# Optimization experiments

Hardware: AMD Instinct MI355X
Metric: run time of the kernel (lower is better)

## Reference

```python
import jax, jax.numpy as jnp
import numpy as np

N_NODES = 150000
N_EDGES = 2400000
IN_DIM, HID, OUT_DIM = 2, 32, 1


def gcn_conv(x, edge_index, W, b, n_nodes):
    """PyG-style GCNConv: add self-loops, sym-normalize, aggregate, linear."""
    h = x @ W  # [N, F_out] linear first (as in PyG GCNConv)
    loop = jnp.arange(n_nodes)
    src = jnp.concatenate([edge_index[0], loop])
    dst = jnp.concatenate([edge_index[1], loop])
    deg = jax.ops.segment_sum(jnp.ones(src.shape[0], h.dtype), dst,
                              num_segments=n_nodes)  # in-degree incl. self-loops
    dinv = jnp.where(deg > 0, jax.lax.rsqrt(deg), 0.0)
    norm = dinv[src] * dinv[dst]  # [E+N]
    msg = h[src] * norm[:, None]  # gather + scale
    out = jax.ops.segment_sum(msg, dst, num_segments=n_nodes)  # scatter-add
    return out + b


def setup_inputs() -> dict:
    key = jax.random.key(0)
    ks = jax.random.split(key, 8)
    x = jax.random.normal(ks[0], (N_NODES, IN_DIM), dtype=jnp.float32)
    edge_index = jax.random.randint(ks[1], (2, N_EDGES), 0, N_NODES, dtype=jnp.int32)
    W1 = jax.random.normal(ks[2], (IN_DIM, HID), dtype=jnp.float32) / np.sqrt(IN_DIM)
    b1 = jnp.zeros((HID,), jnp.float32)
    W2 = jax.random.normal(ks[3], (HID, HID), dtype=jnp.float32) / np.sqrt(HID)
    b2 = jnp.zeros((HID,), jnp.float32)
    Wp = jax.random.normal(ks[4], (HID, OUT_DIM), dtype=jnp.float32) / np.sqrt(HID)
    bp = jnp.zeros((OUT_DIM,), jnp.float32)
    return {"x": x, "edge_index": edge_index, "W1": W1, "b1": b1,
            "W2": W2, "b2": b2, "Wp": Wp, "bp": bp}


def reference(x, edge_index, W1, b1, W2, b2, Wp, bp):
    n = x.shape[0]
    h = jax.nn.relu(gcn_conv(x, edge_index, W1, b1, n))
    h = jax.nn.relu(gcn_conv(h, edge_index, W2, b2, n))
    return jax.nn.sigmoid(h @ Wp + bp)  # [N, 1]
```

## Files before the change

kernel.cpp:

```cpp
#include <hip/hip_runtime.h>

#define HID 32
#define SH 9
#define BNODES 512
#define NBMAX 320
#define TILE 8192

typedef unsigned int uint;

__device__ __forceinline__ uint f2bf(float v) {
    uint b = __float_as_uint(v);
    return (b + 0x7fffu + ((b >> 16) & 1u)) >> 16;
}

__global__ void k_zero(int* __restrict__ p, int n) {
    int i = blockIdx.x * 256 + threadIdx.x;
    if (i < n) p[i] = 0;
}

__global__ void __launch_bounds__(512) k_bcount(const int* __restrict__ dst,
                                                int* __restrict__ bcnt, int E, int NB) {
    __shared__ int c[NBMAX];
    for (int b = threadIdx.x; b < NBMAX; b += 512) c[b] = 0;
    __syncthreads();
    int E4 = E >> 2;
    int b4 = blockIdx.x * (TILE >> 2);
    const int4* dst4 = (const int4*)dst;
#pragma unroll
    for (int k = 0; k < TILE / 4 / 512; ++k) {
        int q = b4 + k * 512 + threadIdx.x;
        if (q < E4) {
            int4 d = dst4[q];
            atomicAdd(&c[d.x >> SH], 1);
            atomicAdd(&c[d.y >> SH], 1);
            atomicAdd(&c[d.z >> SH], 1);
            atomicAdd(&c[d.w >> SH], 1);
        }
    }
    if (blockIdx.x == 0 && threadIdx.x == 0)
        for (int i = E4 << 2; i < E; ++i) atomicAdd(&c[dst[i] >> SH], 1);
    __syncthreads();
    for (int b = threadIdx.x; b < NB; b += 512)
        if (c[b]) atomicAdd(&bcnt[b], c[b]);
}

__global__ void k_scanb(const int* __restrict__ bcnt, int* __restrict__ bbase,
                        int* __restrict__ rowptr, int N, int NB) {
    __shared__ int l[NBMAX + 1];
    int tid = threadIdx.x;
    if (tid < 64) {
        int lo = tid * 5;
        int s = 0;
        for (int b = lo; b < lo + 5 && b < NB; ++b) s += bcnt[b];
        int v = s;
        for (int off = 1; off < 64; off <<= 1) {
            int u = __shfl_up(v, off, 64);
            if (tid >= off) v += u;
        }
        int excl = v - s;
        for (int b = lo; b < lo + 5 && b < NB; ++b) { l[b] = excl; excl += bcnt[b]; }
        if (tid == 63) l[NB] = excl;
    }
    __syncthreads();
    for (int b = tid; b <= NB; b += blockDim.x) bbase[b] = l[b];
    if (tid == 0) rowptr[N] = l[NB];
}

__global__ void __launch_bounds__(512) k_bucketize(
        const int* __restrict__ src, const int* __restrict__ dst,
        const int* __restrict__ bbase, int* __restrict__ bcur,
        uint* __restrict__ ebuf, int E, int NB) {
    __shared__ uint  ecache[TILE];
    __shared__ unsigned short bcache[TILE];
    __shared__ int cnt[NBMAX];
    __shared__ int loff[NBMAX + 1];
    __shared__ int gbase[NBMAX];
    int tid = threadIdx.x;
    int tbase = blockIdx.x * TILE;
    int tcount = min(E - tbase, TILE);
    int tc4 = tcount >> 2;
    const int4* dst4 = (const int4*)(dst + tbase);
    const int4* src4 = (const int4*)(src + tbase);

    for (int b = tid; b < NBMAX; b += 512) cnt[b] = 0;
    __syncthreads();
#pragma unroll
    for (int k = 0; k < TILE / 4 / 512; ++k) {
        int q = k * 512 + tid;
        if (q < tc4) {
            int4 d = dst4[q];
            atomicAdd(&cnt[d.x >> SH], 1);
            atomicAdd(&cnt[d.y >> SH], 1);
            atomicAdd(&cnt[d.z >> SH], 1);
            atomicAdd(&cnt[d.w >> SH], 1);
        }
    }
    if (tid == 0)
        for (int t = tc4 << 2; t < tcount; ++t) atomicAdd(&cnt[dst[tbase + t] >> SH], 1);
    __syncthreads();
    if (tid < 64) {
        int lo = tid * 5;
        int s = 0;
        for (int b = lo; b < lo + 5 && b < NB; ++b) s += cnt[b];
        int v = s;
        for (int off = 1; off < 64; off <<= 1) {
            int u = __shfl_up(v, off, 64);
            if (tid >= off) v += u;
        }
        int excl = v - s;
        for (int b = lo; b < lo + 5 && b < NB; ++b) { loff[b] = excl; excl += cnt[b]; }
        if (tid == 63) loff[NB] = excl;
    }
    __syncthreads();
    for (int b = tid; b < NB; b += 512) cnt[b] = loff[b];
    __syncthreads();
#pragma unroll
    for (int k = 0; k < TILE / 4 / 512; ++k) {
        int q = k * 512 + tid;
        if (q < tc4) {
            int4 d = dst4[q];
            int4 s = src4[q];
            int b0 = d.x >> SH, p0 = atomicAdd(&cnt[b0], 1);
            ecache[p0] = (uint)s.x | ((uint)(d.x & (BNODES - 1)) << 18); bcache[p0] = (unsigned short)b0;
            int b1 = d.y >> SH, p1_ = atomicAdd(&cnt[b1], 1);
            ecache[p1_] = (uint)s.y | ((uint)(d.y & (BNODES - 1)) << 18); bcache[p1_] = (unsigned short)b1;
            int b2 = d.z >> SH, p2_ = atomicAdd(&cnt[b2], 1);
            ecache[p2_] = (uint)s.z | ((uint)(d.z & (BNODES - 1)) << 18); bcache[p2_] = (unsigned short)b2;
            int b3 = d.w >> SH, p3_ = atomicAdd(&cnt[b3], 1);
            ecache[p3_] = (uint)s.w | ((uint)(d.w & (BNODES - 1)) << 18); bcache[p3_] = (unsigned short)b3;
        }
    }
    if (tid == 0)
        for (int t = tc4 << 2; t < tcount; ++t) {
            int d = dst[tbase + t];
            int b_ = d >> SH;
            int pos = atomicAdd(&cnt[b_], 1);
            ecache[pos] = (uint)src[tbase + t] | ((uint)(d & (BNODES - 1)) << 18);
            bcache[pos] = (unsigned short)b_;
        }
    __syncthreads();
    for (int b = tid; b < NB; b += 512) {
        int tc = loff[b + 1] - loff[b];
        if (tc > 0) gbase[b] = bbase[b] + atomicAdd(&bcur[b], tc);
    }
    __syncthreads();
    for (int j = tid; j < tcount; j += 512) {
        int b = bcache[j];
        ebuf[gbase[b] + (j - loff[b])] = ecache[j];
    }
}

__global__ void __launch_bounds__(512) k_sortb(
        const uint* __restrict__ ebuf, const int* __restrict__ bbase,
        const float* __restrict__ x,
        int* __restrict__ rowptr, float* __restrict__ dinv,
        float2* __restrict__ p1, int* __restrict__ col, int N) {
    __shared__ int c[BNODES];
    __shared__ int off[BNODES];
    __shared__ int cur[BNODES];
    int b = blockIdx.x, tid = threadIdx.x;
    int base = bbase[b], cnt = bbase[b + 1] - base;
    for (int t = tid; t < BNODES; t += 512) c[t] = 0;
    __syncthreads();
    int pre = min(cnt, (4 - (base & 3)) & 3);
    for (int j = tid; j < pre; j += 512) atomicAdd(&c[ebuf[base + j] >> 18], 1);
    int vb = base + pre;
    int vc = (cnt - pre) >> 2;
    const uint4* e4 = (const uint4*)(ebuf + vb);
    for (int q = tid; q < vc; q += 512) {
        uint4 e = e4[q];
        atomicAdd(&c[e.x >> 18], 1);
        atomicAdd(&c[e.y >> 18], 1);
        atomicAdd(&c[e.z >> 18], 1);
        atomicAdd(&c[e.w >> 18], 1);
    }
    for (int j = pre + (vc << 2) + tid; j < cnt; j += 512)
        atomicAdd(&c[ebuf[base + j] >> 18], 1);
    __syncthreads();
    if (tid < 64) {
        int lo = tid * 8, s = 0;
#pragma unroll
        for (int k = 0; k < 8; ++k) s += c[lo + k];
        int v = s;
        for (int o = 1; o < 64; o <<= 1) {
            int u = __shfl_up(v, o, 64);
            if (tid >= o) v += u;
        }
        int excl = v - s;
#pragma unroll
        for (int k = 0; k < 8; ++k) { off[lo + k] = excl; excl += c[lo + k]; }
    }
    __syncthreads();
    for (int t = tid; t < BNODES; t += 512) {
        cur[t] = off[t];
        int node = (b << SH) + t;
        if (node < N) {
            rowptr[node] = base + off[t];
            float di = rsqrtf((float)c[t] + 1.0f);
            dinv[node] = di;
            float2 xv = ((const float2*)x)[node];
            p1[node] = make_float2(xv.x * di, xv.y * di);
        }
    }
    __syncthreads();
    for (int j = tid; j < pre; j += 512) {
        uint e = ebuf[base + j];
        int dl = e >> 18;
        int pos = atomicAdd(&cur[dl], 1);
        col[base + pos] = (int)(e & 0x3FFFF);
    }
    for (int q = tid; q < vc; q += 512) {
        uint4 e = e4[q];
        int dl, pos;
        dl = e.x >> 18; pos = atomicAdd(&cur[dl], 1); col[base + pos] = (int)(e.x & 0x3FFFF);
        dl = e.y >> 18; pos = atomicAdd(&cur[dl], 1); col[base + pos] = (int)(e.y & 0x3FFFF);
        dl = e.z >> 18; pos = atomicAdd(&cur[dl], 1); col[base + pos] = (int)(e.z & 0x3FFFF);
        dl = e.w >> 18; pos = atomicAdd(&cur[dl], 1); col[base + pos] = (int)(e.w & 0x3FFFF);
    }
    for (int j = pre + (vc << 2) + tid; j < cnt; j += 512) {
        uint e = ebuf[base + j];
        int dl = e >> 18;
        int pos = atomicAdd(&cur[dl], 1);
        col[base + pos] = (int)(e & 0x3FFFF);
    }
}

__global__ void __launch_bounds__(256) k_gl12(
        const int* __restrict__ rowptr, const int* __restrict__ col,
        const float2* __restrict__ p1, const float* __restrict__ dinv,
        const float* __restrict__ W1, const float* __restrict__ b1,
        const float* __restrict__ W2, uint* __restrict__ p2h, int N) {
    __shared__ float sW1[64], sb1[32], sW2[HID * HID];
    int tid = threadIdx.x;
    for (int t = tid; t < HID * HID; t += 256) sW2[t] = W2[t];
    if (tid < 64) sW1[tid] = W1[tid];
    if (tid < 32) sb1[tid] = b1[tid];
    __syncthreads();
    int i = blockIdx.x * 16 + (tid >> 4);
    if (i >= N) return;
    int sub = tid & 15;

    int beg = rowptr[i], end = rowptr[i + 1];
    float ax = 0, ay = 0, bx = 0, by = 0;
    int j = beg + sub;
    for (; j + 16 < end; j += 32) {
        int c0 = col[j], c1 = col[j + 16];
        float2 v0 = p1[c0], v1 = p1[c1];
        ax += v0.x; ay += v0.y;
        bx += v1.x; by += v1.y;
    }
    if (j < end) {
        float2 v = p1[col[j]];
        ax += v.x; ay += v.y;
    }
    float sx = ax + bx, sy = ay + by;
#pragma unroll
    for (int m = 1; m < 16; m <<= 1) {
        sx += __shfl_xor(sx, m, 16);
        sy += __shfl_xor(sy, m, 16);
    }

    float2 a = p1[i];
    float di = dinv[i];
    float g0 = di * (a.x + sx);
    float g1 = di * (a.y + sy);

    float h0 = fmaxf(g0 * sW1[2 * sub] + g1 * sW1[32 + 2 * sub] + sb1[2 * sub], 0.0f);
    float h1 = fmaxf(g0 * sW1[2 * sub + 1] + g1 * sW1[32 + 2 * sub + 1] + sb1[2 * sub + 1], 0.0f);

    float o0 = 0, o1 = 0;
    int fb = 2 * sub;
#pragma unroll
    for (int s = 0; s < 16; ++s) {
        float hk0 = __shfl(h0, s, 16);
        float hk1 = __shfl(h1, s, 16);
        const float* w0 = &sW2[(2 * s) * HID + fb];
        const float* w1 = &sW2[(2 * s + 1) * HID + fb];
        o0 += hk0 * w0[0]; o1 += hk0 * w0[1];
        o0 += hk1 * w1[0]; o1 += hk1 * w1[1];
    }

    p2h[(long)i * 16 + sub] = f2bf(di * o0) | (f2bf(di * o1) << 16);
}

__global__ void k_gout(const int* __restrict__ rowptr, const int* __restrict__ col,
                       const uint* __restrict__ p2h, const float* __restrict__ b2,
                       const float* __restrict__ Wp, const float* __restrict__ bp,
                       const float* __restrict__ dinv, float* __restrict__ out, int N) {
    int node = blockIdx.x * 16 + (threadIdx.x >> 4);
    if (node >= N) return;
    int hl = threadIdx.x & 15;
    int beg = rowptr[node], end = rowptr[node + 1];
    uint w = p2h[(long)node * 16 + hl];
    float sA0 = __uint_as_float(w << 16), sB0 = __uint_as_float(w & 0xffff0000u);
    float sA1 = 0, sB1 = 0, sA2 = 0, sB2 = 0, sA3 = 0, sB3 = 0;
    int j = beg;
    for (; j + 4 <= end; j += 4) {
        int c0 = col[j], c1 = col[j + 1], c2 = col[j + 2], c3 = col[j + 3];
        uint w0 = p2h[(long)c0 * 16 + hl];
        uint w1 = p2h[(long)c1 * 16 + hl];
        uint w2 = p2h[(long)c2 * 16 + hl];
        uint w3 = p2h[(long)c3 * 16 + hl];
        sA0 += __uint_as_float(w0 << 16); sB0 += __uint_as_float(w0 & 0xffff0000u);
        sA1 += __uint_as_float(w1 << 16); sB1 += __uint_as_float(w1 & 0xffff0000u);
        sA2 += __uint_as_float(w2 << 16); sB2 += __uint_as_float(w2 & 0xffff0000u);
        sA3 += __uint_as_float(w3 << 16); sB3 += __uint_as_float(w3 & 0xffff0000u);
    }
    for (; j < end; ++j) {
        uint wj = p2h[(long)col[j] * 16 + hl];
        sA0 += __uint_as_float(wj << 16); sB0 += __uint_as_float(wj & 0xffff0000u);
    }
    float sA = (sA0 + sA1) + (sA2 + sA3);
    float sB = (sB0 + sB1) + (sB2 + sB3);
    float di = dinv[node];
    float hvA = fmaxf(di * sA + b2[2 * hl], 0.0f);
    float hvB = fmaxf(di * sB + b2[2 * hl + 1], 0.0f);
    float v = hvA * Wp[2 * hl] + hvB * Wp[2 * hl + 1];
#pragma unroll
    for (int m = 8; m > 0; m >>= 1) v += __shfl_xor(v, m, 16);
    if (hl == 0) out[node] = 1.0f / (1.0f + expf(-(v + bp[0])));
}

extern "C" void kernel_launch(void* const* d_in, const int* in_sizes, int n_in,
                              void* d_out, int out_size, void* d_ws, size_t ws_size,
                              hipStream_t stream) {
    const float* x  = (const float*)d_in[0];
    const int*   ei = (const int*)d_in[1];
    const float* W1 = (const float*)d_in[2];
    const float* b1 = (const float*)d_in[3];
    const float* W2 = (const float*)d_in[4];
    const float* b2 = (const float*)d_in[5];
    const float* Wp = (const float*)d_in[6];
    const float* bp = (const float*)d_in[7];
    float* out = (float*)d_out;

    const int N = in_sizes[0] / 2;
    const int E = in_sizes[1] / 2;
    const int* src = ei;
    const int* dst = ei + E;
    const int NB = (N + BNODES - 1) >> SH;

    char* ws = (char*)d_ws;
    size_t off = 0;
    auto alloc = [&](size_t bytes) {
        void* ptr = ws + off;
        off += (bytes + 255) & ~(size_t)255;
        return ptr;
    };
    int*    bcnt   = (int*)alloc((size_t)NBMAX * 4);
    int*    bcur   = (int*)alloc((size_t)NBMAX * 4);
    int*    bbase  = (int*)alloc((size_t)(NBMAX + 1) * 4);
    int*    rowptr = (int*)alloc((size_t)(N + 1) * 4);
    float*  dinv   = (float*)alloc((size_t)N * 4);
    uint*   ebuf   = (uint*)alloc((size_t)E * 4);
    int*    col    = (int*)alloc((size_t)E * 4);
    float2* p1     = (float2*)alloc((size_t)N * 8);
    uint*   p2h    = (uint*)alloc((size_t)N * 16 * 4);

    const int nb_t = (E + TILE - 1) / TILE;
    const int nb_g = (N + 15) / 16;
    const int nb_16 = (N + 15) / 16;

    k_zero<<<(2 * NBMAX + 255) / 256, 256, 0, stream>>>(bcnt, 2 * NBMAX);
    k_bcount<<<nb_t, 512, 0, stream>>>(dst, bcnt, E, NB);
    k_scanb<<<1, 256, 0, stream>>>(bcnt, bbase, rowptr, N, NB);
    k_bucketize<<<nb_t, 512, 0, stream>>>(src, dst, bbase, bcur, ebuf, E, NB);
    k_sortb<<<NB, 512, 0, stream>>>(ebuf, bbase, x, rowptr, dinv, p1, col, N);
    k_gl12<<<nb_g, 256, 0, stream>>>(rowptr, col, p1, dinv, W1, b1, W2, p2h, N);
    k_gout<<<nb_16, 256, 0, stream>>>(rowptr, col, p2h, b2, Wp, bp, dinv, out, N);
}
```

Measured before the change: 128.4 us.

## Drop bucket count pass with fixed-capacity bucket slots and LDS staging

Removes the separate destination-bucket counting kernel. k_bucketize now writes each bucket into a fixed-capacity slot (CAP entries per bucket), and the per-bucket totals come from the atomic cursors, which are scanned afterwards. k_sortb stages each bucket's edges in shared memory so the second pass reads LDS instead of global memory. This saves one full read of dst and a launch, but assumes no bucket exceeds CAP edges and raises k_sortb's shared-memory footprint, which lowers its occupancy.

```diff
diff --git a/kernel.cpp b/kernel.cpp
--- a/kernel.cpp
+++ b/kernel.cpp
@@ -5,6 +5,8 @@
 #define BNODES 512
 #define NBMAX 320
 #define TILE 8192
+#define CAP 16384
+#define STAGECAP 12288
 
 typedef unsigned int uint;
 
@@ -18,58 +20,9 @@
     if (i < n) p[i] = 0;
 }
 
-__global__ void __launch_bounds__(512) k_bcount(const int* __restrict__ dst,
-                                                int* __restrict__ bcnt, int E, int NB) {
-    __shared__ int c[NBMAX];
-    for (int b = threadIdx.x; b < NBMAX; b += 512) c[b] = 0;
-    __syncthreads();
-    int E4 = E >> 2;
-    int b4 = blockIdx.x * (TILE >> 2);
-    const int4* dst4 = (const int4*)dst;
-#pragma unroll
-    for (int k = 0; k < TILE / 4 / 512; ++k) {
-        int q = b4 + k * 512 + threadIdx.x;
-        if (q < E4) {
-            int4 d = dst4[q];
-            atomicAdd(&c[d.x >> SH], 1);
-            atomicAdd(&c[d.y >> SH], 1);
-            atomicAdd(&c[d.z >> SH], 1);
-            atomicAdd(&c[d.w >> SH], 1);
-        }
-    }
-    if (blockIdx.x == 0 && threadIdx.x == 0)
-        for (int i = E4 << 2; i < E; ++i) atomicAdd(&c[dst[i] >> SH], 1);
-    __syncthreads();
-    for (int b = threadIdx.x; b < NB; b += 512)
-        if (c[b]) atomicAdd(&bcnt[b], c[b]);
-}
-
-__global__ void k_scanb(const int* __restrict__ bcnt, int* __restrict__ bbase,
-                        int* __restrict__ rowptr, int N, int NB) {
-    __shared__ int l[NBMAX + 1];
-    int tid = threadIdx.x;
-    if (tid < 64) {
-        int lo = tid * 5;
-        int s = 0;
-        for (int b = lo; b < lo + 5 && b < NB; ++b) s += bcnt[b];
-        int v = s;
-        for (int off = 1; off < 64; off <<= 1) {
-            int u = __shfl_up(v, off, 64);
-            if (tid >= off) v += u;
-        }
-        int excl = v - s;
-        for (int b = lo; b < lo + 5 && b < NB; ++b) { l[b] = excl; excl += bcnt[b]; }
-        if (tid == 63) l[NB] = excl;
-    }
-    __syncthreads();
-    for (int b = tid; b <= NB; b += blockDim.x) bbase[b] = l[b];
-    if (tid == 0) rowptr[N] = l[NB];
-}
-
 __global__ void __launch_bounds__(512) k_bucketize(
         const int* __restrict__ src, const int* __restrict__ dst,
-        const int* __restrict__ bbase, int* __restrict__ bcur,
-        uint* __restrict__ ebuf, int E, int NB) {
+        int* __restrict__ bcur, uint* __restrict__ ebuf, int E, int NB) {
     __shared__ uint  ecache[TILE];
     __shared__ unsigned short bcache[TILE];
     __shared__ int cnt[NBMAX];
@@ -141,7 +94,7 @@
     __syncthreads();
     for (int b = tid; b < NB; b += 512) {
         int tc = loff[b + 1] - loff[b];
-        if (tc > 0) gbase[b] = bbase[b] + atomicAdd(&bcur[b], tc);
+        if (tc > 0) gbase[b] = b * CAP + atomicAdd(&bcur[b], tc);
     }
     __syncthreads();
     for (int j = tid; j < tcount; j += 512) {
@@ -150,32 +103,61 @@
     }
 }
 
+__global__ void k_scanb(const int* __restrict__ bcur, int* __restrict__ bbase,
+                        int* __restrict__ rowptr, int N, int NB) {
+    __shared__ int l[NBMAX + 1];
+    int tid = threadIdx.x;
+    if (tid < 64) {
+        int lo = tid * 5;
+        int s = 0;
+        for (int b = lo; b < lo + 5 && b < NB; ++b) s += bcur[b];
+        int v = s;
+        for (int off = 1; off < 64; off <<= 1) {
+            int u = __shfl_up(v, off, 64);
+            if (tid >= off) v += u;
+        }
+        int excl = v - s;
+        for (int b = lo; b < lo + 5 && b < NB; ++b) { l[b] = excl; excl += bcur[b]; }
+        if (tid == 63) l[NB] = excl;
+    }
+    __syncthreads();
+    for (int b = tid; b <= NB; b += blockDim.x) bbase[b] = l[b];
+    if (tid == 0) rowptr[N] = l[NB];
+}
+
 __global__ void __launch_bounds__(512) k_sortb(
-        const uint* __restrict__ ebuf, const int* __restrict__ bbase,
-        const float* __restrict__ x,
+        const uint* __restrict__ ebuf, const int* __restrict__ bcur,
+        const int* __restrict__ bbase, const float* __restrict__ x,
         int* __restrict__ rowptr, float* __restrict__ dinv,
         float2* __restrict__ p1, int* __restrict__ col, int N) {
     __shared__ int c[BNODES];
     __shared__ int off[BNODES];
     __shared__ int cur[BNODES];
+    __shared__ uint stage[STAGECAP];
     int b = blockIdx.x, tid = threadIdx.x;
-    int base = bbase[b], cnt = bbase[b + 1] - base;
+    int cnt = bcur[b];
+    const uint* eb = ebuf + (long)b * CAP;
+    int cbase = bbase[b];
     for (int t = tid; t < BNODES; t += 512) c[t] = 0;
     __syncthreads();
-    int pre = min(cnt, (4 - (base & 3)) & 3);
-    for (int j = tid; j < pre; j += 512) atomicAdd(&c[ebuf[base + j] >> 18], 1);
-    int vb = base + pre;
-    int vc = (cnt - pre) >> 2;
-    const uint4* e4 = (const uint4*)(ebuf + vb);
+    int vc = cnt >> 2;
+    const uint4* e4 = (const uint4*)eb;
     for (int q = tid; q < vc; q += 512) {
         uint4 e = e4[q];
         atomicAdd(&c[e.x >> 18], 1);
         atomicAdd(&c[e.y >> 18], 1);
         atomicAdd(&c[e.z >> 18], 1);
         atomicAdd(&c[e.w >> 18], 1);
-    }
-    for (int j = pre + (vc << 2) + tid; j < cnt; j += 512)
-        atomicAdd(&c[ebuf[base + j] >> 18], 1);
+        int j = q << 2;
+        if (j + 3 < STAGECAP) {
+            stage[j] = e.x; stage[j + 1] = e.y; stage[j + 2] = e.z; stage[j + 3] = e.w;
+        }
+    }
+    for (int j = (vc << 2) + tid; j < cnt; j += 512) {
+        uint e = eb[j];
+        atomicAdd(&c[e >> 18], 1);
+        if (j < STAGECAP) stage[j] = e;
+    }
     __syncthreads();
     if (tid < 64) {
         int lo = tid * 8, s = 0;
@@ -195,7 +177,7 @@
         cur[t] = off[t];
         int node = (b << SH) + t;
         if (node < N) {
-            rowptr[node] = base + off[t];
+            rowptr[node] = cbase + off[t];
             float di = rsqrtf((float)c[t] + 1.0f);
             dinv[node] = di;
             float2 xv = ((const float2*)x)[node];
@@ -203,25 +185,18 @@
         }
     }
     __syncthreads();
-    for (int j = tid; j < pre; j += 512) {
-        uint e = ebuf[base + j];
+    int lim = min(cnt, STAGECAP);
+    for (int j = tid; j < lim; j += 512) {
+        uint e = stage[j];
         int dl = e >> 18;
         int pos = atomicAdd(&cur[dl], 1);
-        col[base + pos] = (int)(e & 0x3FFFF);
-    }
-    for (int q = tid; q < vc; q += 512) {
-        uint4 e = e4[q];
-        int dl, pos;
-        dl = e.x >> 18; pos = atomicAdd(&cur[dl], 1); col[base + pos] = (int)(e.x & 0x3FFFF);
-        dl = e.y >> 18; pos = atomicAdd(&cur[dl], 1); col[base + pos] = (int)(e.y & 0x3FFFF);
-        dl = e.z >> 18; pos = atomicAdd(&cur[dl], 1); col[base + pos] = (int)(e.z & 0x3FFFF);
-        dl = e.w >> 18; pos = atomicAdd(&cur[dl], 1); col[base + pos] = (int)(e.w & 0x3FFFF);
-    }
-    for (int j = pre + (vc << 2) + tid; j < cnt; j += 512) {
-        uint e = ebuf[base + j];
+        col[cbase + pos] = (int)(e & 0x3FFFF);
+    }
+    for (int j = STAGECAP + tid; j < cnt; j += 512) {
+        uint e = eb[j];
         int dl = e >> 18;
         int pos = atomicAdd(&cur[dl], 1);
-        col[base + pos] = (int)(e & 0x3FFFF);
+        col[cbase + pos] = (int)(e & 0x3FFFF);
     }
 }
 
@@ -347,25 +322,22 @@
         off += (bytes + 255) & ~(size_t)255;
         return ptr;
     };
-    int*    bcnt   = (int*)alloc((size_t)NBMAX * 4);
     int*    bcur   = (int*)alloc((size_t)NBMAX * 4);
     int*    bbase  = (int*)alloc((size_t)(NBMAX + 1) * 4);
     int*    rowptr = (int*)alloc((size_t)(N + 1) * 4);
     float*  dinv   = (float*)alloc((size_t)N * 4);
-    uint*   ebuf   = (uint*)alloc((size_t)E * 4);
+    uint*   ebuf   = (uint*)alloc((size_t)NBMAX * CAP * 4);
     int*    col    = (int*)alloc((size_t)E * 4);
     float2* p1     = (float2*)alloc((size_t)N * 8);
     uint*   p2h    = (uint*)alloc((size_t)N * 16 * 4);
 
     const int nb_t = (E + TILE - 1) / TILE;
     const int nb_g = (N + 15) / 16;
-    const int nb_16 = (N + 15) / 16;
-
-    k_zero<<<(2 * NBMAX + 255) / 256, 256, 0, stream>>>(bcnt, 2 * NBMAX);
-    k_bcount<<<nb_t, 512, 0, stream>>>(dst, bcnt, E, NB);
-    k_scanb<<<1, 256, 0, stream>>>(bcnt, bbase, rowptr, N, NB);
-    k_bucketize<<<nb_t, 512, 0, stream>>>(src, dst, bbase, bcur, ebuf, E, NB);
-    k_sortb<<<NB, 512, 0, stream>>>(ebuf, bbase, x, rowptr, dinv, p1, col, N);
+
+    k_zero<<<(NBMAX + 255) / 256, 256, 0, stream>>>(bcur, NBMAX);
+    k_bucketize<<<nb_t, 512, 0, stream>>>(src, dst, bcur, ebuf, E, NB);
+    k_scanb<<<1, 256, 0, stream>>>(bcur, bbase, rowptr, N, NB);
+    k_sortb<<<NB, 512, 0, stream>>>(ebuf, bcur, bbase, x, rowptr, dinv, p1, col, N);
     k_gl12<<<nb_g, 256, 0, stream>>>(rowptr, col, p1, dinv, W1, b1, W2, p2h, N);
-    k_gout<<<nb_16, 256, 0, stream>>>(rowptr, col, p2h, b2, Wp, bp, dinv, out, N);
-}
+    k_gout<<<nb_g, 256, 0, stream>>>(rowptr, col, p2h, b2, Wp, bp, dinv, out, N);
+}
```

After: 120.6 us. -6.1%, faster.
